# Optimization experiments

Measured on AMD Instinct MI355X. Metric: run time of the kernel, lower is better.

Reference implementation:

```python
import jax, jax.numpy as jnp
import numpy as np

B, D_MODEL, H, D_MEM, M = 512, 2048, 8, 128, 512
MAX_WRITE_FACTOR = 0.7


def act(x):
    # elu(x) + 1, the standard positive linear-attention kernel activation
    return jax.nn.elu(x) + 1.0


def setup_inputs() -> dict:
    key = jax.random.key(0)
    ks = jax.random.split(key, 9)
    s = 1.0 / np.sqrt(D_MODEL)
    return {
        "key": jax.random.normal(ks[0], (B, D_MODEL), jnp.float32),
        "values": jax.random.normal(ks[1], (B, D_MODEL), jnp.float32),
        "memories": jax.random.normal(ks[2], (B, M, D_MEM), jnp.float32),
        "write_mass": jax.random.uniform(ks[3], (B, M, D_MEM), jnp.float32),
        "batch_mask": jnp.zeros((B,), jnp.bool_),
        "W_key": jax.random.normal(ks[4], (D_MODEL, H * D_MEM), jnp.float32) * s,
        "b_key": jnp.zeros((H * D_MEM,), jnp.float32),
        "W_val": jax.random.normal(ks[5], (D_MODEL, 2 * H * D_MEM), jnp.float32) * s,
        "b_val": jnp.zeros((2 * H * D_MEM,), jnp.float32),
        "addresses": jax.random.normal(ks[6], (M, D_MEM), jnp.float32),
        "interpolation_logits": jax.random.normal(ks[7], (M, D_MEM), jnp.float32),
    }


def reference(key, values, memories, write_mass, batch_mask,
              W_key, b_key, W_val, b_val, addresses, interpolation_logits):
    # project write heads
    k = (key @ W_key + b_key).reshape(B, H, D_MEM)            # (B, H, Dm)
    v = (values @ W_val + b_val).reshape(B, H, 2 * D_MEM)     # (B, H, 2Dm)

    # linear attention kernel over heads (items = H)
    ak = act(k)
    matrix = jnp.einsum('bhd,bhe->bde', ak, v)                 # (B, Dm, 2Dm)
    normalizer = jnp.sum(ak, axis=1)                           # (B, Dm)

    # read with memory addresses as queries
    aq = act(addresses)                                        # (M, Dm)
    numerator = jnp.einsum('md,bde->bme', aq, matrix)          # (B, M, 2Dm)
    denominator = jnp.einsum('md,bd->bm', aq, normalizer) + 1e-5
    results = numerator / denominator[..., None]

    update = results[..., :D_MEM]                              # (B, M, Dm)
    write_logits = results[..., D_MEM:]                        # (B, M, Dm)

    write_probability = jax.nn.sigmoid(write_logits)
    interpolation_factor = jax.nn.sigmoid(interpolation_logits)  # (M, Dm)
    write_factor = MAX_WRITE_FACTOR * write_probability * interpolation_factor

    # probability-gated EMA-style commit
    next_memories = memories * (1.0 - write_factor) + update * write_factor
    next_mass = write_mass + write_factor

    mask = batch_mask[:, None, None]
    next_memories = jnp.where(mask, memories, next_memories)
    next_mass = jnp.where(mask, write_mass, next_mass)
    return next_memories, next_mass
```

## Files before the change

### kernel.cpp

```cpp
#include <hip/hip_runtime.h>


typedef _Float16 half8  __attribute__((ext_vector_type(8)));
typedef _Float16 half4v __attribute__((ext_vector_type(4)));
typedef float    f32x4  __attribute__((ext_vector_type(4)));

#define NB      512
#define DMODEL  2048
#define NH      8
#define DMEM    128
#define NM      512
#define NMTOT   33554432

__device__ __forceinline__ f32x4 ntload4(const float* p) {
    return __builtin_nontemporal_load((const f32x4*)p);
}
__device__ __forceinline__ void ntstore4(float* p, f32x4 v) {
    __builtin_nontemporal_store(v, (f32x4*)p);
}

__global__ void cvt_f32_f16(const float* __restrict__ in, _Float16* __restrict__ out, int n4) {
    int i = blockIdx.x * blockDim.x + threadIdx.x;
    if (i < n4) {
        float4 v = ((const float4*)in)[i];
        half4v o;
        o[0] = (_Float16)v.x; o[1] = (_Float16)v.y;
        o[2] = (_Float16)v.z; o[3] = (_Float16)v.w;
        ((half4v*)out)[i] = o;
    }
}

__global__ void transp_cvt(const float* __restrict__ W, _Float16* __restrict__ Wt, int N) {
    __shared__ float tile[32][33];
    const int k0 = blockIdx.x * 32, n0 = blockIdx.y * 32;
    const int c = threadIdx.x & 31, r0 = threadIdx.x >> 5;
#pragma unroll
    for (int i = 0; i < 4; i++) {
        int r = r0 + i * 8;
        tile[r][c] = W[(size_t)(k0 + r) * N + n0 + c];
    }
    __syncthreads();
#pragma unroll
    for (int i = 0; i < 4; i++) {
        int r = r0 + i * 8;
        Wt[(size_t)(n0 + r) * 2048 + k0 + c] = (_Float16)tile[c][r];
    }
}

__global__ void prep_aq(const float* __restrict__ addresses, const float* __restrict__ ilog,
                        float* __restrict__ aqF, _Float16* __restrict__ aqH,
                        float* __restrict__ sigI) {
    int i = blockIdx.x * 256 + threadIdx.x;
    float a = addresses[i];
    float v = a > 0.f ? a + 1.f : __expf(a);
    aqF[i] = v;
    aqH[i] = (_Float16)v;
    sigI[i] = 1.0f / (1.0f + __expf(-ilog[i]));
}

__global__ __launch_bounds__(256) void gemm_kv(
        const _Float16* __restrict__ key16,
        const _Float16* __restrict__ val16,
        const _Float16* __restrict__ WkT,
        const _Float16* __restrict__ WvT,
        const float* __restrict__ b_key,
        const float* __restrict__ b_val,
        float* __restrict__ akF,
        _Float16* __restrict__ vH) {
    __shared__ _Float16 As[2][64][72];
    __shared__ _Float16 Bs[2][64][72];

    const int t = threadIdx.x;
    const int m0 = blockIdx.x * 64;
    const int n0 = blockIdx.y * 64;
    const bool isK = (n0 < 1024);
    const _Float16* aSrc = isK ? key16 : val16;
    const _Float16* bSrc = isK ? (WkT + (size_t)n0 * 2048)
                               : (WvT + (size_t)(n0 - 1024) * 2048);

    const int w = t >> 6, lane = t & 63;
    const int col = lane & 15, q = lane >> 4;
    const int wm = (w & 1) * 32, wn = (w >> 1) * 32;

    const int row0 = t >> 3, ch = t & 7;
    const int row1 = (t + 256) >> 3;

    f32x4 acc[2][2];
#pragma unroll
    for (int i = 0; i < 2; i++)
#pragma unroll
        for (int j = 0; j < 2; j++) acc[i][j] = (f32x4){0.f, 0.f, 0.f, 0.f};

    uint4 ra0 = *(const uint4*)(aSrc + (size_t)(m0 + row0) * 2048 + ch * 8);
    uint4 ra1 = *(const uint4*)(aSrc + (size_t)(m0 + row1) * 2048 + ch * 8);
    uint4 rb0 = *(const uint4*)(bSrc + (size_t)row0 * 2048 + ch * 8);
    uint4 rb1 = *(const uint4*)(bSrc + (size_t)row1 * 2048 + ch * 8);

    int buf = 0;
    for (int k0 = 0; k0 < 2048; k0 += 64) {
        *(uint4*)&As[buf][row0][ch * 8] = ra0;
        *(uint4*)&As[buf][row1][ch * 8] = ra1;
        *(uint4*)&Bs[buf][row0][ch * 8] = rb0;
        *(uint4*)&Bs[buf][row1][ch * 8] = rb1;
        if (k0 + 64 < 2048) {
            const int kn = k0 + 64;
            ra0 = *(const uint4*)(aSrc + (size_t)(m0 + row0) * 2048 + kn + ch * 8);
            ra1 = *(const uint4*)(aSrc + (size_t)(m0 + row1) * 2048 + kn + ch * 8);
            rb0 = *(const uint4*)(bSrc + (size_t)row0 * 2048 + kn + ch * 8);
            rb1 = *(const uint4*)(bSrc + (size_t)row1 * 2048 + kn + ch * 8);
        }
        __syncthreads();
#pragma unroll
        for (int ks = 0; ks < 2; ks++) {
            half8 a0 = *(const half8*)&As[buf][wm + col][ks * 32 + q * 8];
            half8 a1 = *(const half8*)&As[buf][wm + 16 + col][ks * 32 + q * 8];
            half8 b0 = *(const half8*)&Bs[buf][wn + col][ks * 32 + q * 8];
            half8 b1 = *(const half8*)&Bs[buf][wn + 16 + col][ks * 32 + q * 8];
            acc[0][0] = __builtin_amdgcn_mfma_f32_16x16x32_f16(a0, b0, acc[0][0], 0, 0, 0);
            acc[0][1] = __builtin_amdgcn_mfma_f32_16x16x32_f16(a0, b1, acc[0][1], 0, 0, 0);
            acc[1][0] = __builtin_amdgcn_mfma_f32_16x16x32_f16(a1, b0, acc[1][0], 0, 0, 0);
            acc[1][1] = __builtin_amdgcn_mfma_f32_16x16x32_f16(a1, b1, acc[1][1], 0, 0, 0);
        }
        buf ^= 1;
    }
#pragma unroll
    for (int mt = 0; mt < 2; mt++) {
#pragma unroll
        for (int nt = 0; nt < 2; nt++) {
            int n = n0 + wn + nt * 16 + col;
#pragma unroll
            for (int r = 0; r < 4; r++) {
                int m = m0 + wm + mt * 16 + q * 4 + r;
                float x = acc[mt][nt][r];
                if (isK) {
                    x += b_key[n];
                    akF[(size_t)m * 1024 + n] = (x > 0.f) ? (x + 1.f) : __expf(x);
                } else {
                    int nn = n - 1024;
                    x += b_val[nn];
                    vH[(size_t)m * 2048 + nn] = (_Float16)x;
                }
            }
        }
    }
}

struct PFBuf { f32x4 pm[2]; f32x4 pw[2]; f32x4 ps[2]; };

__global__ __launch_bounds__(1024, 1) void fused_mem(
    const float* __restrict__ akF,
    const _Float16* __restrict__ vH,
    const _Float16* __restrict__ aqH,
    const float* __restrict__ aqF,
    const float* __restrict__ sigI,
    const float* __restrict__ memories,
    const float* __restrict__ write_mass,
    const unsigned char* __restrict__ bmask,
    float* __restrict__ out) {
    __shared__ _Float16 matT[256][DMEM + 8];
    __shared__ float    uT[64][132];
    __shared__ float    gT[64][132];
    __shared__ float    sA[NH][DMEM];
    __shared__ _Float16 sV[NH][256];
    __shared__ float    sNrm[DMEM];
    __shared__ float    sDen[NM];

    const int b = blockIdx.x;
    const int t = threadIdx.x;
    const int w = t >> 6, lane = t & 63;
    const int col = lane & 15, q = lane >> 4;
    const int wq = w >> 2, slice = w & 3;
    const int lr = lane >> 5, e4 = (lane & 31) * 4;
    const size_t obase = (size_t)b * (NM * DMEM);

    PFBuf A, B;

    auto pf_issue = [&](PFBuf& pb, int s) {
        const int mrow = (wq + (s >> 2) * 4) * 64 + (s & 3) * 16 + slice * 4 + lr;
#pragma unroll
        for (int p = 0; p < 2; p++) {
            const size_t gi = (size_t)(mrow + p * 2) * 128 + e4;
            pb.pm[p] = ntload4(memories + obase + gi);
            pb.pw[p] = ntload4(write_mass + obase + gi);
            pb.ps[p] = *(const f32x4*)(sigI + gi);
        }
    };

    pf_issue(A, 0);

    if (t < 256) {
        ((float4*)&sA[0][0])[t] = ((const float4*)(akF + (size_t)b * 1024))[t];
        ((uint4*)&sV[0][0])[t]  = ((const uint4*)(vH + (size_t)b * 2048))[t];
    }
    __syncthreads();

    if (t < 128) {
        float s = 0.f;
#pragma unroll
        for (int h = 0; h < NH; h++) s += sA[h][t];
        sNrm[t] = s;
    }

    {
        const int d0 = (t & 31) * 4;
        const int e0 = (t >> 5) * 8;
        float c[8][4];
#pragma unroll
        for (int e = 0; e < 8; e++)
#pragma unroll
            for (int d = 0; d < 4; d++) c[e][d] = 0.f;
#pragma unroll
        for (int h = 0; h < NH; h++) {
            float4 av = *(const float4*)&sA[h][d0];
            half8 vv = *(const half8*)&sV[h][e0];
#pragma unroll
            for (int e = 0; e < 8; e++) {
                float vf = (float)vv[e];
                c[e][0] += av.x * vf; c[e][1] += av.y * vf;
                c[e][2] += av.z * vf; c[e][3] += av.w * vf;
            }
        }
#pragma unroll
        for (int e = 0; e < 8; e++) {
            half4v o;
            o[0] = (_Float16)c[e][0]; o[1] = (_Float16)c[e][1];
            o[2] = (_Float16)c[e][2]; o[3] = (_Float16)c[e][3];
            *(half4v*)&matT[e0 + e][d0] = o;
        }
    }
    __syncthreads();

    {
        const int l32 = lane & 31;
        const int hh = lane >> 5;
        const float4 nv = *(const float4*)&sNrm[l32 * 4];
#pragma unroll 4
        for (int pass = 0; pass < 16; pass++) {
            int m = pass * 32 + w * 2 + hh;
            float4 qv = *(const float4*)(aqF + (size_t)m * 128 + l32 * 4);
            float s = qv.x * nv.x + qv.y * nv.y + qv.z * nv.z + qv.w * nv.w;
            s += __shfl_xor(s, 1);  s += __shfl_xor(s, 2);  s += __shfl_xor(s, 4);
            s += __shfl_xor(s, 8);  s += __shfl_xor(s, 16);
            if (l32 == 0) sDen[m] = 1.0f / (s + 1e-5f);
        }
    }
    __syncthreads();

    const float wfscale = (bmask[b] != 0) ? 0.0f : 0.7f;

    auto do_step = [&](int s, PFBuf& cur, PFBuf& nxt) {
        if (s < 7) pf_issue(nxt, s + 1);

        const int mrowBase = (wq + (s >> 2) * 4) * 64 + (s & 3) * 16;
        f32x4 acc[4];
#pragma unroll
        for (int nt = 0; nt < 4; nt++) acc[nt] = (f32x4){0.f, 0.f, 0.f, 0.f};
#pragma unroll
        for (int ks = 0; ks < 4; ks++) {
            const half8 af = *(const half8*)(aqH + (size_t)(mrowBase + col) * 128
                                             + ks * 32 + q * 8);
#pragma unroll
            for (int nt = 0; nt < 4; nt++) {
                const half8 bf = *(const half8*)&matT[slice * 32 + (nt & 1) * 16
                                                      + (nt >> 1) * 128 + col]
                                                     [ks * 32 + q * 8];
                acc[nt] = __builtin_amdgcn_mfma_f32_16x16x32_f16(af, bf, acc[nt], 0, 0, 0);
            }
        }

        asm volatile("s_waitcnt lgkmcnt(0)" ::: "memory");
        __builtin_amdgcn_s_barrier();
        __builtin_amdgcn_sched_barrier(0);

        const int r0 = wq * 16 + q * 4;
#pragma unroll
        for (int r = 0; r < 4; r++) {
            uT[r0 + r][slice * 32 + col]      = acc[0][r];
            uT[r0 + r][slice * 32 + 16 + col] = acc[1][r];
            gT[r0 + r][slice * 32 + col]      = acc[2][r];
            gT[r0 + r][slice * 32 + 16 + col] = acc[3][r];
        }

        asm volatile("s_waitcnt lgkmcnt(0)" ::: "memory");
        __builtin_amdgcn_s_barrier();
        __builtin_amdgcn_sched_barrier(0);

#pragma unroll
        for (int p = 0; p < 2; p++) {
            const int row = w * 4 + p * 2 + lr;
            const int m = mrowBase + slice * 4 + p * 2 + lr;
            const f32x4 u = *(const f32x4*)&uT[row][e4];
            const f32x4 g = *(const f32x4*)&gT[row][e4];
            const float rc = sDen[m];
            const size_t gi = obase + (size_t)m * 128 + e4;
            f32x4 o1, o2;
#pragma unroll
            for (int j = 0; j < 4; j++) {
                const float upd = u[j] * rc;
                const float wl  = g[j] * rc;
                const float wpb = 1.0f / (1.0f + __expf(-wl));
                const float wf  = wfscale * wpb * cur.ps[p][j];
                o1[j] = cur.pm[p][j] + wf * (upd - cur.pm[p][j]);
                o2[j] = cur.pw[p][j] + wf;
            }
            ntstore4(out + gi, o1);
            ntstore4(out + NMTOT + gi, o2);
        }
    };

    for (int s2 = 0; s2 < 8; s2 += 2) {
        do_step(s2,     A, B);
        do_step(s2 + 1, B, A);
    }
}

extern "C" void kernel_launch(void* const* d_in, const int* in_sizes, int n_in,
                              void* d_out, int out_size, void* d_ws, size_t ws_size,
                              hipStream_t stream) {
    const float* key        = (const float*)d_in[0];
    const float* values     = (const float*)d_in[1];
    const float* memories   = (const float*)d_in[2];
    const float* write_mass = (const float*)d_in[3];
    const unsigned char* bm = (const unsigned char*)d_in[4];
    const float* W_key      = (const float*)d_in[5];
    const float* b_key      = (const float*)d_in[6];
    const float* W_val      = (const float*)d_in[7];
    const float* b_val      = (const float*)d_in[8];
    const float* addresses  = (const float*)d_in[9];
    const float* ilog       = (const float*)d_in[10];
    float* out = (float*)d_out;

    char* ws = (char*)d_ws;
    _Float16* key16 = (_Float16*)ws;  ws += (size_t)512 * 2048 * 2;
    _Float16* val16 = (_Float16*)ws;  ws += (size_t)512 * 2048 * 2;
    _Float16* WkT   = (_Float16*)ws;  ws += (size_t)1024 * 2048 * 2;
    _Float16* WvT   = (_Float16*)ws;  ws += (size_t)2048 * 2048 * 2;
    float*    akF   = (float*)ws;     ws += (size_t)512 * 1024 * 4;
    _Float16* vH    = (_Float16*)ws;  ws += (size_t)512 * 2048 * 2;
    float*    aqF   = (float*)ws;     ws += (size_t)512 * 128 * 4;
    _Float16* aqH   = (_Float16*)ws;  ws += (size_t)512 * 128 * 2;
    float*    sigI  = (float*)ws;     ws += (size_t)512 * 128 * 4;

    cvt_f32_f16<<<1024, 256, 0, stream>>>(key, key16, 262144);
    cvt_f32_f16<<<1024, 256, 0, stream>>>(values, val16, 262144);
    transp_cvt<<<dim3(64, 32), 256, 0, stream>>>(W_key, WkT, 1024);
    transp_cvt<<<dim3(64, 64), 256, 0, stream>>>(W_val, WvT, 2048);
    prep_aq<<<256, 256, 0, stream>>>(addresses, ilog, aqF, aqH, sigI);
    gemm_kv<<<dim3(8, 48), 256, 0, stream>>>(key16, val16, WkT, WvT, b_key, b_val, akF, vH);
    fused_mem<<<512, 1024, 0, stream>>>(akF, vH, aqH, aqF, sigI, memories, write_mass, bm, out);
}
```

Baseline: 544.0 us.

## Split fused memory kernel over two e-column halves per batch

Splits the fused_mem grid across two blocks per batch. Each block has 512 threads and handles 64 of the 128 e-columns, which halves its shared-memory tiles and lets several blocks reside per CU under launch bounds (512,4). The aim is better occupancy and latency hiding for the bandwidth-bound streaming of memories and write_mass. The cost is that each block recomputes the normalizer and the full 512-entry denominator, and the output store pattern per row becomes narrower (64-column segments).

```diff
diff --git a/kernel.cpp b/kernel.cpp
--- a/kernel.cpp
+++ b/kernel.cpp
@@ -147,7 +147,7 @@
 
 struct PFBuf { f32x4 pm[2]; f32x4 pw[2]; f32x4 ps[2]; };
 
-__global__ __launch_bounds__(1024, 1) void fused_mem(
+__global__ __launch_bounds__(512, 4) void fused_mem(
     const float* __restrict__ akF,
     const _Float16* __restrict__ vH,
     const _Float16* __restrict__ aqH,
@@ -157,29 +157,33 @@
     const float* __restrict__ write_mass,
     const unsigned char* __restrict__ bmask,
     float* __restrict__ out) {
-    __shared__ _Float16 matT[256][DMEM + 8];
-    __shared__ float    uT[64][132];
-    __shared__ float    gT[64][132];
+    __shared__ _Float16 matT[128][DMEM + 8];
+    __shared__ float    uT[64][68];
+    __shared__ float    gT[64][68];
     __shared__ float    sA[NH][DMEM];
-    __shared__ _Float16 sV[NH][256];
+    __shared__ _Float16 sV[NH][128];
     __shared__ float    sNrm[DMEM];
     __shared__ float    sDen[NM];
 
-    const int b = blockIdx.x;
+    const int b  = blockIdx.x;
+    const int eh = blockIdx.y;
     const int t = threadIdx.x;
     const int w = t >> 6, lane = t & 63;
     const int col = lane & 15, q = lane >> 4;
-    const int wq = w >> 2, slice = w & 3;
-    const int lr = lane >> 5, e4 = (lane & 31) * 4;
+    const int wq = w >> 1, slice = w & 1;
     const size_t obase = (size_t)b * (NM * DMEM);
+    const int ebase = eh * 64;
 
     PFBuf A, B;
 
     auto pf_issue = [&](PFBuf& pb, int s) {
-        const int mrow = (wq + (s >> 2) * 4) * 64 + (s & 3) * 16 + slice * 4 + lr;
+        const int it = s >> 2, mt = s & 3;
+        const int e4 = ebase + (lane & 15) * 4;
 #pragma unroll
         for (int p = 0; p < 2; p++) {
-            const size_t gi = (size_t)(mrow + p * 2) * 128 + e4;
+            const int x = w * 8 + p * 4 + (lane >> 4);
+            const int m = (x >> 4) * 64 + it * 256 + mt * 16 + (x & 15);
+            const size_t gi = (size_t)m * 128 + e4;
             pb.pm[p] = ntload4(memories + obase + gi);
             pb.pw[p] = ntload4(write_mass + obase + gi);
             pb.ps[p] = *(const f32x4*)(sigI + gi);
@@ -190,7 +194,11 @@
 
     if (t < 256) {
         ((float4*)&sA[0][0])[t] = ((const float4*)(akF + (size_t)b * 1024))[t];
-        ((uint4*)&sV[0][0])[t]  = ((const uint4*)(vH + (size_t)b * 2048))[t];
+    }
+    if (t < 128) {
+        const int h = t >> 4, grp = t & 15;
+        const int eg = (grp < 8) ? (ebase + grp * 8) : (128 + ebase + (grp - 8) * 8);
+        *(half8*)&sV[h][grp * 8] = *(const half8*)(vH + (size_t)b * 2048 + h * 256 + eg);
     }
     __syncthreads();
 
@@ -235,8 +243,8 @@
         const int hh = lane >> 5;
         const float4 nv = *(const float4*)&sNrm[l32 * 4];
 #pragma unroll 4
-        for (int pass = 0; pass < 16; pass++) {
-            int m = pass * 32 + w * 2 + hh;
+        for (int pass = 0; pass < 32; pass++) {
+            int m = pass * 16 + w * 2 + hh;
             float4 qv = *(const float4*)(aqF + (size_t)m * 128 + l32 * 4);
             float s = qv.x * nv.x + qv.y * nv.y + qv.z * nv.z + qv.w * nv.w;
             s += __shfl_xor(s, 1);  s += __shfl_xor(s, 2);  s += __shfl_xor(s, 4);
@@ -251,7 +259,8 @@
     auto do_step = [&](int s, PFBuf& cur, PFBuf& nxt) {
         if (s < 7) pf_issue(nxt, s + 1);
 
-        const int mrowBase = (wq + (s >> 2) * 4) * 64 + (s & 3) * 16;
+        const int it = s >> 2, mt = s & 3;
+        const int mrowBase = (wq + it * 4) * 64 + mt * 16;
         f32x4 acc[4];
 #pragma unroll
         for (int nt = 0; nt < 4; nt++) acc[nt] = (f32x4){0.f, 0.f, 0.f, 0.f};
@@ -261,8 +270,8 @@
                                              + ks * 32 + q * 8);
 #pragma unroll
             for (int nt = 0; nt < 4; nt++) {
-                const half8 bf = *(const half8*)&matT[slice * 32 + (nt & 1) * 16
-                                                      + (nt >> 1) * 128 + col]
+                const half8 bf = *(const half8*)&matT[(nt >> 1) * 64 + slice * 32
+                                                      + (nt & 1) * 16 + col]
                                                      [ks * 32 + q * 8];
                 acc[nt] = __builtin_amdgcn_mfma_f32_16x16x32_f16(af, bf, acc[nt], 0, 0, 0);
             }
@@ -285,14 +294,15 @@
         __builtin_amdgcn_s_barrier();
         __builtin_amdgcn_sched_barrier(0);
 
+        const int e4l = (lane & 15) * 4;
 #pragma unroll
         for (int p = 0; p < 2; p++) {
-            const int row = w * 4 + p * 2 + lr;
-            const int m = mrowBase + slice * 4 + p * 2 + lr;
-            const f32x4 u = *(const f32x4*)&uT[row][e4];
-            const f32x4 g = *(const f32x4*)&gT[row][e4];
+            const int x = w * 8 + p * 4 + (lane >> 4);
+            const int m = (x >> 4) * 64 + it * 256 + mt * 16 + (x & 15);
+            const f32x4 u = *(const f32x4*)&uT[x][e4l];
+            const f32x4 g = *(const f32x4*)&gT[x][e4l];
             const float rc = sDen[m];
-            const size_t gi = obase + (size_t)m * 128 + e4;
+            const size_t gi = obase + (size_t)m * 128 + ebase + e4l;
             f32x4 o1, o2;
 #pragma unroll
             for (int j = 0; j < 4; j++) {
@@ -347,5 +357,5 @@
     transp_cvt<<<dim3(64, 64), 256, 0, stream>>>(W_val, WvT, 2048);
     prep_aq<<<256, 256, 0, stream>>>(addresses, ilog, aqF, aqH, sigI);
     gemm_kv<<<dim3(8, 48), 256, 0, stream>>>(key16, val16, WkT, WvT, b_key, b_val, akF, vH);
-    fused_mem<<<512, 1024, 0, stream>>>(akF, vH, aqH, aqF, sigI, memories, write_mass, bm, out);
-}
+    fused_mem<<<dim3(512, 2), 512, 0, stream>>>(akF, vH, aqH, aqF, sigI, memories, write_mass, bm, out);
+}
```

New measurement: 545.6 us. About the same (+0.3%).
